# Kernel optimization log

Measured on AMD Instinct MI355X. Metric: run time of the kernel, lower is better.

Reference implementation:

```python
import jax, jax.numpy as jnp
import numpy as np

N = 50000      # nodes
E = 800000     # edges
D = 64         # model dim (in_dim == out_dim)
H = 8          # heads
Dh = D // H    # head dim = 8
CLAMP = 5.0
EPS_BN = 1e-5


def setup_inputs() -> dict:
    key = jax.random.key(0)
    ks = jax.random.split(key, 16)
    g = lambda i, shape, s=0.1: (jax.random.normal(ks[i], shape, jnp.float32) * s)
    z = lambda shape: jnp.zeros(shape, jnp.float32)
    o = lambda shape: jnp.ones(shape, jnp.float32)
    return dict(
        x=g(0, (N, D), 1.0),
        edge_attr=g(1, (E, D), 1.0),
        edge_index=jax.random.randint(ks[2], (2, E), 0, N, jnp.int32),
        Wq=g(3, (D, H * Dh)), bq=z((H * Dh,)),
        Wk=g(4, (D, H * Dh)),                      # K: use_bias=False (cfg default)
        We=g(5, (D, 2 * H * Dh)), be=z((2 * H * Dh,)),
        Wv=g(6, (D, H * Dh)),                      # V: use_bias=False
        Aw=g(7, (Dh, H, 1)),
        VeRow=g(8, (Dh, H, Dh)),
        deg_coef=g(9, (1, D, 2)),
        WOh=g(10, (D, D)), bOh=z((D,)),
        WOe=g(11, (D, D)), bOe=z((D,)),
        gamma1h=o((D,)), beta1h=z((D,)),
        gamma1e=o((D,)), beta1e=z((D,)),
        W1=g(12, (D, 2 * D)), b1=z((2 * D,)),
        W2=g(13, (2 * D, D)), b2=z((D,)),
        gamma2h=o((D,)), beta2h=z((D,)),
    )


def _bn(v, gamma, beta):
    # BatchNorm1d with batch statistics (training-mode math, biased var as in torch)
    mu = v.mean(axis=0)
    var = ((v - mu) ** 2).mean(axis=0)
    return (v - mu) * jax.lax.rsqrt(var + EPS_BN) * gamma + beta


def reference(x, edge_attr, edge_index, Wq, bq, Wk, We, be, Wv, Aw, VeRow,
              deg_coef, WOh, bOh, WOe, bOe, gamma1h, beta1h, gamma1e, beta1e,
              W1, b1, W2, b2, gamma2h, beta2h):
    src, dst = edge_index[0], edge_index[1]
    # degree scaler: deg computed on the fly from edge_index[1]
    deg = jax.ops.segment_sum(jnp.ones((E,), x.dtype), dst, num_segments=N)
    log_deg = jnp.log(deg + 1.0)[:, None]                       # [N,1]

    Q = (x @ Wq + bq).reshape(N, H, Dh)
    K = (x @ Wk).reshape(N, H, Dh)
    V = (x @ Wv).reshape(N, H, Dh)
    Ee = (edge_attr @ We + be).reshape(E, H, 2 * Dh)
    Ew, Eb = Ee[:, :, :Dh], Ee[:, :, Dh:]

    s = (K[src] + Q[dst]) * Ew                                  # [E,H,Dh]
    s = jnp.sqrt(jax.nn.relu(s)) - jnp.sqrt(jax.nn.relu(-s))    # signed sqrt
    s = jax.nn.relu(s + Eb)                                     # attn act = relu
    e_t = s
    wE = s.reshape(E, H * Dh)

    score = jnp.einsum('ehd,dhc->ehc', s, Aw)                   # [E,H,1]
    score = jnp.clip(score, -CLAMP, CLAMP)
    # segment softmax over destination nodes
    m = jax.ops.segment_max(score, dst, num_segments=N)
    m = jnp.where(jnp.isfinite(m), m, 0.0)
    ex = jnp.exp(score - m[dst])
    denom = jax.ops.segment_sum(ex, dst, num_segments=N)
    attn = ex / (denom[dst] + 1e-16)                            # [E,H,1]

    wV = jax.ops.segment_sum(V[src] * attn, dst, num_segments=N)    # [N,H,Dh]
    rowV = jax.ops.segment_sum(e_t * attn, dst, num_segments=N)     # [N,H,Dh]
    wV = wV + jnp.einsum('nhd,dhc->nhc', rowV, VeRow)

    h = wV.reshape(N, H * Dh)
    h = h * deg_coef[:, :, 0] + (h * log_deg) * deg_coef[:, :, 1]
    h = h @ WOh + bOh
    e = wE @ WOe + bOe

    h = _bn(x + h, gamma1h, beta1h)
    e = _bn(edge_attr + e, gamma1e, beta1e)

    h2 = jax.nn.relu(h @ W1 + b1) @ W2 + b2
    h = _bn(h + h2, gamma2h, beta2h)
    return h, e
```

## Files before the change

### kernel.cpp

```cpp
#include <hip/hip_runtime.h>
#include <hip/hip_bf16.h>

#define N_NODES 50000
#define N_EDGES 800000
#define CLAMP_V 5.0f
#define MAXDEG 64

typedef __hip_bfloat16 bf16;
typedef short s16x8 __attribute__((ext_vector_type(8)));
typedef float f32x4 __attribute__((ext_vector_type(4)));

__device__ __forceinline__ float b2f(bf16 v){ return __bfloat162float(v); }
__device__ __forceinline__ bf16 f2b(float v){ return __float2bfloat16(v); }

__device__ __forceinline__ float ldin(const void* p, size_t i, bool f32){
  return f32 ? ((const float*)p)[i] : b2f(((const bf16*)p)[i]);
}
__device__ __forceinline__ void stout(void* p, size_t i, float v, bool f32){
  if(f32) ((float*)p)[i]=v; else ((bf16*)p)[i]=f2b(v);
}
__device__ __forceinline__ void* e_region(void* d_out, bool f32){
  return f32 ? (void*)((float*)d_out + (size_t)N_NODES*64)
             : (void*)((bf16*)d_out + (size_t)N_NODES*64);
}

#define W_FLAG 0
#define W_DEG  64
#define W_ST   50064
#define W_ZEND 50448
#define W_BUCK 50448
#define W_QK   6450448
#define W_V    12850448
#define W_END  16050448
#define W_HV   W_QK
#define W_HPRE W_BUCK
#define W_HSUM (W_BUCK+3200000)

__global__ void detect_kernel(const unsigned short* __restrict__ wq_raw, unsigned* __restrict__ flag){
  int t=threadIdx.x; int cnt=0;
  for(int i=t;i<4096;i+=64){
    unsigned e=(wq_raw[i]>>7)&0xFF;
    if(e>=130) cnt++;
  }
  for(int o=32;o;o>>=1) cnt+=__shfl_down(cnt,o);
  if(t==0) *flag = (cnt>64)? 1u:0u;
}

__global__ __launch_bounds__(256) void build_kernel(const int* __restrict__ edge_index,
    unsigned* __restrict__ deg, uint2* __restrict__ buck2)
{
  int e = blockIdx.x*256+threadIdx.x;
  if(e < N_EDGES){
    int src = edge_index[e];
    int dst = edge_index[N_EDGES+e];
    unsigned j = atomicAdd(&deg[dst],1u);
    if(j < MAXDEG) buck2[(size_t)dst*MAXDEG + j] = make_uint2((unsigned)e,(unsigned)src);
  }
}

__global__ __launch_bounds__(256) void qkv_kernel(const void* __restrict__ x,
    const void* __restrict__ Wq, const void* __restrict__ bq,
    const void* __restrict__ Wk, const void* __restrict__ Wv,
    const unsigned* __restrict__ flagp, float* __restrict__ qk, float* __restrict__ vbuf)
{
  const bool f = (*flagp)!=0;
  __shared__ float sW[64*192];
  __shared__ float4 sxT[4][64];
  int t=threadIdx.x, wave=t>>6, lane=t&63;
  for (int i=t;i<64*64;i+=256){ int k=i>>6, j=i&63;
    sW[k*192+j]=ldin(Wq,i,f); sW[k*192+64+j]=ldin(Wk,i,f); sW[k*192+128+j]=ldin(Wv,i,f); }
  float bqv = ldin(bq,lane,f);
  __syncthreads();
  const int groups = N_NODES/16;
  const int stride = gridDim.x;
  int g = blockIdx.x;
  float cv0=0,cv1=0,cv2=0,cv3=0;
  if(g<groups){
    int n0=g*16+wave*4;
    cv0=ldin(x,(size_t)(n0+0)*64+lane,f);
    cv1=ldin(x,(size_t)(n0+1)*64+lane,f);
    cv2=ldin(x,(size_t)(n0+2)*64+lane,f);
    cv3=ldin(x,(size_t)(n0+3)*64+lane,f);
  }
  for (; g<groups; g+=stride){
    int n0 = g*16 + wave*4;
    sxT[wave][lane]=make_float4(cv0,cv1,cv2,cv3);
    int gn=g+stride; int gl = gn<groups?gn:g; int m0=gl*16+wave*4;
    float nv0=ldin(x,(size_t)(m0+0)*64+lane,f);
    float nv1=ldin(x,(size_t)(m0+1)*64+lane,f);
    float nv2=ldin(x,(size_t)(m0+2)*64+lane,f);
    float nv3=ldin(x,(size_t)(m0+3)*64+lane,f);
    float aq[4]={0,0,0,0}, ak[4]={0,0,0,0}, av[4]={0,0,0,0};
    #pragma unroll 8
    for(int k=0;k<64;k++){
      float4 a = sxT[wave][k];
      float w0=sW[k*192+lane], w1=sW[k*192+64+lane], w2=sW[k*192+128+lane];
      aq[0]+=a.x*w0; aq[1]+=a.y*w0; aq[2]+=a.z*w0; aq[3]+=a.w*w0;
      ak[0]+=a.x*w1; ak[1]+=a.y*w1; ak[2]+=a.z*w1; ak[3]+=a.w*w1;
      av[0]+=a.x*w2; av[1]+=a.y*w2; av[2]+=a.z*w2; av[3]+=a.w*w2;
    }
    #pragma unroll
    for(int r=0;r<4;r++){
      int n=n0+r;
      qk[n*128+lane]     = aq[r]+bqv;
      qk[n*128+64+lane]  = ak[r];
      vbuf[n*64+lane]    = av[r];
    }
    cv0=nv0; cv1=nv1; cv2=nv2; cv3=nv3;
  }
}

__global__ __launch_bounds__(256) void edgeA_kernel(
    const void* __restrict__ edge_attr, const int* __restrict__ edge_index,
    const void* __restrict__ We, const void* __restrict__ be,
    const float* __restrict__ qk, const unsigned* __restrict__ flagp, void* __restrict__ d_out)
{
  const bool f = (*flagp)!=0;
  void* s_buf = e_region(d_out,f);
  __shared__ float2 sWWB[64*64];
  __shared__ float4 seaT[4][64];
  int t=threadIdx.x, wave=t>>6, lane=t&63;
  int h=lane>>3, d=lane&7;
  for(int i=t;i<64*64;i+=256){ int k=i>>6, c=i&63; int hh=c>>3, dd=c&7;
    sWWB[i]=make_float2(ldin(We,(size_t)k*128+hh*16+dd,f),
                        ldin(We,(size_t)k*128+hh*16+8+dd,f)); }
  float beW=ldin(be,h*16+d,f), beB=ldin(be,h*16+8+d,f);
  __syncthreads();
  const int groups = N_EDGES/16;
  const int stride = gridDim.x;
  int g = blockIdx.x;
  if(g>=groups) return;
  float cv0,cv1,cv2,cv3; int cs0,cs1,cs2,cs3, cd0,cd1,cd2,cd3;
  {
    int e0=g*16+wave*4;
    cv0=ldin(edge_attr,(size_t)(e0+0)*64+lane,f);
    cv1=ldin(edge_attr,(size_t)(e0+1)*64+lane,f);
    cv2=ldin(edge_attr,(size_t)(e0+2)*64+lane,f);
    cv3=ldin(edge_attr,(size_t)(e0+3)*64+lane,f);
    cs0=edge_index[e0+0]; cs1=edge_index[e0+1]; cs2=edge_index[e0+2]; cs3=edge_index[e0+3];
    cd0=edge_index[N_EDGES+e0+0]; cd1=edge_index[N_EDGES+e0+1];
    cd2=edge_index[N_EDGES+e0+2]; cd3=edge_index[N_EDGES+e0+3];
  }
  for(; g<groups; g+=stride){
    int e0 = g*16 + wave*4;
    seaT[wave][lane]=make_float4(cv0,cv1,cv2,cv3);
    float kS0=qk[(size_t)cs0*128+64+lane], kD0=qk[(size_t)cd0*128+lane];
    float kS1=qk[(size_t)cs1*128+64+lane], kD1=qk[(size_t)cd1*128+lane];
    float kS2=qk[(size_t)cs2*128+64+lane], kD2=qk[(size_t)cd2*128+lane];
    float kS3=qk[(size_t)cs3*128+64+lane], kD3=qk[(size_t)cd3*128+lane];
    int gn=g+stride; int gl = gn<groups?gn:g; int m0=gl*16+wave*4;
    float nv0=ldin(edge_attr,(size_t)(m0+0)*64+lane,f);
    float nv1=ldin(edge_attr,(size_t)(m0+1)*64+lane,f);
    float nv2=ldin(edge_attr,(size_t)(m0+2)*64+lane,f);
    float nv3=ldin(edge_attr,(size_t)(m0+3)*64+lane,f);
    int ns0=edge_index[m0+0], ns1=edge_index[m0+1], ns2=edge_index[m0+2], ns3=edge_index[m0+3];
    int nd0=edge_index[N_EDGES+m0+0], nd1=edge_index[N_EDGES+m0+1];
    int nd2=edge_index[N_EDGES+m0+2], nd3=edge_index[N_EDGES+m0+3];
    float aW[4]={0,0,0,0}, aB[4]={0,0,0,0};
    #pragma unroll 8
    for(int k=0;k<64;k++){
      float4 a=seaT[wave][k];
      float2 w=sWWB[k*64+lane];
      aW[0]+=a.x*w.x; aB[0]+=a.x*w.y;
      aW[1]+=a.y*w.x; aB[1]+=a.y*w.y;
      aW[2]+=a.z*w.x; aB[2]+=a.z*w.y;
      aW[3]+=a.w*w.x; aB[3]+=a.w*w.y;
    }
    float kq0=kS0+kD0, kq1=kS1+kD1, kq2=kS2+kD2, kq3=kS3+kD3;
    {
      float Ew=aW[0]+beW, Eb=aB[0]+beB, s1=kq0*Ew;
      float s2=fmaxf(copysignf(sqrtf(fabsf(s1)),s1)+Eb,0.f);
      stout(s_buf,(size_t)(e0+0)*64+lane,s2,f);
    }
    {
      float Ew=aW[1]+beW, Eb=aB[1]+beB, s1=kq1*Ew;
      float s2=fmaxf(copysignf(sqrtf(fabsf(s1)),s1)+Eb,0.f);
      stout(s_buf,(size_t)(e0+1)*64+lane,s2,f);
    }
    {
      float Ew=aW[2]+beW, Eb=aB[2]+beB, s1=kq2*Ew;
      float s2=fmaxf(copysignf(sqrtf(fabsf(s1)),s1)+Eb,0.f);
      stout(s_buf,(size_t)(e0+2)*64+lane,s2,f);
    }
    {
      float Ew=aW[3]+beW, Eb=aB[3]+beB, s1=kq3*Ew;
      float s2=fmaxf(copysignf(sqrtf(fabsf(s1)),s1)+Eb,0.f);
      stout(s_buf,(size_t)(e0+3)*64+lane,s2,f);
    }
    cv0=nv0; cv1=nv1; cv2=nv2; cv3=nv3;
    cs0=ns0; cs1=ns1; cs2=ns2; cs3=ns3;
    cd0=nd0; cd1=nd1; cd2=nd2; cd3=nd3;
  }
}

__global__ __launch_bounds__(256) void gather_kernel(
    const unsigned* __restrict__ deg, const uint2* __restrict__ buck2,
    const void* __restrict__ Aw, const void* __restrict__ VeRow, const void* __restrict__ deg_coef,
    const float* __restrict__ vbuf, const unsigned* __restrict__ flagp,
    void* __restrict__ d_out, float* __restrict__ hv)
{
  const bool f = (*flagp)!=0;
  const void* s_buf = e_region(d_out,f);
  int t=threadIdx.x, wave=t>>6, lane=t&63;
  int h=lane>>3, d=lane&7;
  float awv = ldin(Aw, d*8+h, f);
  float ver[8];
  #pragma unroll
  for(int dd=0;dd<8;dd++) ver[dd]=ldin(VeRow,(dd*8+h)*8+d,f);
  float dc0=ldin(deg_coef,lane*2,f), dc1=ldin(deg_coef,lane*2+1,f);

  int n = blockIdx.x*4 + wave;
  unsigned degree = deg[n];
  int len = (int)(degree < MAXDEG ? degree : MAXDEG);
  const uint2* bk = &buck2[(size_t)n*MAXDEG];

  float den=0.f, wv=0.f, rv=0.f;
  for(int j=0;j<len;j+=4){
    float sv[4], vq[4]; int valid[4];
    #pragma unroll
    for(int i=0;i<4;i++){
      int jj=j+i; int js = jj<len ? jj : len-1;
      uint2 es = bk[js];
      sv[i]=ldin(s_buf,(size_t)es.x*64+lane,f);
      vq[i]=vbuf[(size_t)es.y*64+lane];
      valid[i]=(jj<len);
    }
    #pragma unroll
    for(int i=0;i<4;i++){
      float p = sv[i]*awv;
      p += __shfl_xor(p,1);
      p += __shfl_xor(p,2);
      p += __shfl_xor(p,4);
      p = fminf(fmaxf(p,-CLAMP_V),CLAMP_V);
      float ex = valid[i] ? __expf(p-CLAMP_V) : 0.f;
      den += ex; wv += vq[i]*ex; rv += sv[i]*ex;
    }
  }
  float inv = 1.f/(den + 1e-16f);
  wv *= inv; rv *= inv;
  float rvp=0.f;
  #pragma unroll
  for(int dd=0;dd<8;dd++){
    float rvd = __shfl(rv, (lane & 56) + dd);
    rvp += rvd * ver[dd];
  }
  float ld = __logf((float)degree + 1.f);
  hv[(size_t)n*64+lane] = (wv + rvp) * (dc0 + ld*dc1);
}

__global__ __launch_bounds__(256) void edgeD_kernel(const void* __restrict__ edge_attr,
    const void* __restrict__ WOe, const void* __restrict__ bOe,
    const unsigned* __restrict__ flagp, void* __restrict__ d_out, float* __restrict__ stats)
{
  const bool f = (*flagp)!=0;
  __shared__ float4 sm4[1536];
  float* sm=(float*)sm4;
  int t=threadIdx.x, wave=t>>6, lane=t&63;
  if(!f){
    bf16* eio = (bf16*)d_out + (size_t)N_NODES*64;
    const unsigned short* sb=(const unsigned short*)eio;
    unsigned short* BT=(unsigned short*)sm;
    float* red = sm + 2048;
    if(t<128) red[t]=0.f;
    for(int i=t;i<4096;i+=256){
      int j=i>>6, k=i&63;
      BT[(j*128+((k*2)^((j&7)<<4)))>>1]=((const unsigned short*)WOe)[(size_t)k*64+j];
    }
    __syncthreads();
    int qg=lane>>4, col=lane&15;
    s16x8 Bf[4][2];
    #pragma unroll
    for(int tl=0;tl<4;tl++){
      int j=tl*16+col;
      #pragma unroll
      for(int q=0;q<2;q++){
        int kb=qg*8+q*32;
        Bf[tl][q]=*(const s16x8*)((const char*)BT+j*128+((kb*2)^((j&7)<<4)));
      }
    }
    float boV[4];
    #pragma unroll
    for(int tl=0;tl<4;tl++) boV[tl]=b2f(((const bf16*)bOe)[tl*16+col]);
    float st1[4]={0,0,0,0}, st2[4]={0,0,0,0};
    f32x4 zz; zz[0]=0.f; zz[1]=0.f; zz[2]=0.f; zz[3]=0.f;
    const int groups=N_EDGES/64;
    for(int g=blockIdx.x; g<groups; g+=gridDim.x){
      int e0=g*64+wave*16, eq=e0+qg*4;
      const unsigned short* apr = sb + (size_t)(e0+col)*64 + qg*8;
      s16x8 A0=*(const s16x8*)apr;
      s16x8 A1=*(const s16x8*)(apr+32);
      f32x4 acc[4];
      #pragma unroll
      for(int tl=0;tl<4;tl++){
        acc[tl]=__builtin_amdgcn_mfma_f32_16x16x32_bf16(A0,Bf[tl][0],zz,0,0,0);
        acc[tl]=__builtin_amdgcn_mfma_f32_16x16x32_bf16(A1,Bf[tl][1],acc[tl],0,0,0);
      }
      #pragma unroll
      for(int r=0;r<4;r++){
        size_t eo=(size_t)(eq+r)*64;
        #pragma unroll
        for(int tl=0;tl<4;tl++){
          int c=tl*16+col;
          float ep=b2f(((const bf16*)edge_attr)[eo+c])+boV[tl]+acc[tl][r];
          eio[eo+c]=f2b(ep);
          st1[tl]+=ep; st2[tl]+=ep*ep;
        }
      }
    }
    #pragma unroll
    for(int tl=0;tl<4;tl++){
      int c=tl*16+col;
      atomicAdd(&red[c],st1[tl]);
      atomicAdd(&red[64+c],st2[tl]);
    }
    __syncthreads();
    if(t<128) atomicAdd(&stats[t],red[t]);
  } else {
    void* e_io = e_region(d_out,f);
    float* sW=sm; float4* sTa=(float4*)(sm+4096); float4* sTb=(float4*)(sm+5120);
    for(int i=t;i<64*64;i+=256) sW[i]=ldin(WOe,i,f);
    float bo=ldin(bOe,lane,f);
    float s1=0.f,s2=0.f;
    __syncthreads();
    const int groups=N_EDGES/32;
    for(int g=blockIdx.x;g<groups;g+=gridDim.x){
      int e0=g*32+wave*8;
      float v[8];
      #pragma unroll
      for(int r=0;r<8;r++) v[r]=ldin(e_io,(size_t)(e0+r)*64+lane,f);
      sTa[wave*64+lane]=make_float4(v[0],v[1],v[2],v[3]);
      sTb[wave*64+lane]=make_float4(v[4],v[5],v[6],v[7]);
      float acc[8]={0,0,0,0,0,0,0,0};
      #pragma unroll 8
      for(int k=0;k<64;k++){
        float4 a=sTa[wave*64+k], b=sTb[wave*64+k];
        float w=sW[k*64+lane];
        acc[0]+=a.x*w; acc[1]+=a.y*w; acc[2]+=a.z*w; acc[3]+=a.w*w;
        acc[4]+=b.x*w; acc[5]+=b.y*w; acc[6]+=b.z*w; acc[7]+=b.w*w;
      }
      #pragma unroll
      for(int r=0;r<8;r++){
        int e=e0+r;
        float ep=ldin(edge_attr,(size_t)e*64+lane,f)+bo+acc[r];
        stout(e_io,(size_t)e*64+lane,ep,f);
        s1+=ep; s2+=ep*ep;
      }
    }
    atomicAdd(&stats[lane], s1);
    atomicAdd(&stats[64+lane], s2);
  }
}

__global__ __launch_bounds__(256) void edgeE_kernel(const unsigned* __restrict__ flagp,
    void* __restrict__ d_out, const float* __restrict__ stats,
    const void* __restrict__ g1e, const void* __restrict__ b1e)
{
  const bool f = (*flagp)!=0;
  void* e_io = e_region(d_out,f);
  size_t tid=(size_t)blockIdx.x*256+threadIdx.x;
  int c=(int)(tid&63);
  float mu=stats[c]*(1.f/N_EDGES);
  float var=stats[64+c]*(1.f/N_EDGES)-mu*mu;
  float rs=rsqrtf(var+1e-5f);
  float val=ldin(e_io,tid,f);
  val=(val-mu)*rs*ldin(g1e,c,f)+ldin(b1e,c,f);
  stout(e_io,tid,val,f);
}

__global__ __launch_bounds__(256) void h1_kernel(const float* __restrict__ hv,
    const void* __restrict__ WOh, const void* __restrict__ bOh, const void* __restrict__ x,
    const unsigned* __restrict__ flagp, float* __restrict__ hpre, float* __restrict__ stats)
{
  const bool f = (*flagp)!=0;
  __shared__ float sW[64*64];
  __shared__ float4 sT[4][64];
  int t=threadIdx.x, wave=t>>6, lane=t&63;
  for(int i=t;i<64*64;i+=256) sW[i]=ldin(WOh,i,f);
  float bo=ldin(bOh,lane,f);
  float s1=0.f,s2=0.f;
  __syncthreads();
  const int groups=N_NODES/16;
  for(int g=blockIdx.x;g<groups;g+=gridDim.x){
    int n0=g*16+wave*4;
    sT[wave][lane]=make_float4(hv[(n0+0)*64+lane],hv[(n0+1)*64+lane],
                               hv[(n0+2)*64+lane],hv[(n0+3)*64+lane]);
    float acc[4]={0,0,0,0};
    #pragma unroll 8
    for(int k=0;k<64;k++){
      float4 a=sT[wave][k]; float w=sW[k*64+lane];
      acc[0]+=a.x*w; acc[1]+=a.y*w; acc[2]+=a.z*w; acc[3]+=a.w*w;
    }
    #pragma unroll
    for(int r=0;r<4;r++){
      int n=n0+r;
      float hp=ldin(x,(size_t)n*64+lane,f)+bo+acc[r];
      hpre[n*64+lane]=hp;
      s1+=hp; s2+=hp*hp;
    }
  }
  atomicAdd(&stats[128+lane],s1);
  atomicAdd(&stats[192+lane],s2);
}

__global__ __launch_bounds__(256) void h2_kernel(const float* __restrict__ hpre,
    const void* __restrict__ W1, const void* __restrict__ b1, const void* __restrict__ W2, const void* __restrict__ b2,
    const void* __restrict__ g1h, const void* __restrict__ be1h,
    const unsigned* __restrict__ flagp, float* __restrict__ hsum, float* __restrict__ stats)
{
  const bool f = (*flagp)!=0;
  __shared__ float sW1[64*128];
  __shared__ float4 shT[4][64];
  __shared__ float4 stT[4][128];
  int t=threadIdx.x, wave=t>>6, lane=t&63;
  for(int i=t;i<64*128;i+=256) sW1[i]=ldin(W1,i,f);
  float mu=stats[128+lane]*(1.f/N_NODES);
  float var=stats[192+lane]*(1.f/N_NODES)-mu*mu;
  float rs=rsqrtf(var+1e-5f);
  float gg=ldin(g1h,lane,f), bb=ldin(be1h,lane,f);
  float b1a=ldin(b1,lane,f), b1b=ldin(b1,64+lane,f);
  float b2c=ldin(b2,lane,f);
  float s1=0.f,s2=0.f;
  __syncthreads();
  const int groups=N_NODES/16;
  for(int g=blockIdx.x;g<groups;g+=gridDim.x){
    int n0=g*16+wave*4;
    float h1v[4];
    #pragma unroll
    for(int r=0;r<4;r++) h1v[r]=(hpre[(n0+r)*64+lane]-mu)*rs*gg+bb;
    shT[wave][lane]=make_float4(h1v[0],h1v[1],h1v[2],h1v[3]);
    float t0[4]={0,0,0,0}, t1[4]={0,0,0,0};
    #pragma unroll 8
    for(int k=0;k<64;k++){
      float4 a=shT[wave][k];
      float w0=sW1[k*128+lane], w1=sW1[k*128+64+lane];
      t0[0]+=a.x*w0; t0[1]+=a.y*w0; t0[2]+=a.z*w0; t0[3]+=a.w*w0;
      t1[0]+=a.x*w1; t1[1]+=a.y*w1; t1[2]+=a.z*w1; t1[3]+=a.w*w1;
    }
    #pragma unroll
    for(int r=0;r<4;r++){ t0[r]=fmaxf(t0[r]+b1a,0.f); t1[r]=fmaxf(t1[r]+b1b,0.f); }
    stT[wave][lane]=make_float4(t0[0],t0[1],t0[2],t0[3]);
    stT[wave][64+lane]=make_float4(t1[0],t1[1],t1[2],t1[3]);
    float acc[4]={0,0,0,0};
    #pragma unroll 8
    for(int k=0;k<128;k++){
      float4 a=stT[wave][k];
      float w=ldin(W2,(size_t)k*64+lane,f);
      acc[0]+=a.x*w; acc[1]+=a.y*w; acc[2]+=a.z*w; acc[3]+=a.w*w;
    }
    #pragma unroll
    for(int r=0;r<4;r++){
      float hs=h1v[r]+acc[r]+b2c;
      hsum[(n0+r)*64+lane]=hs;
      s1+=hs; s2+=hs*hs;
    }
  }
  atomicAdd(&stats[256+lane],s1);
  atomicAdd(&stats[320+lane],s2);
}

__global__ __launch_bounds__(256) void h3_kernel(const float* __restrict__ hsum,
    const float* __restrict__ stats, const void* __restrict__ g2h, const void* __restrict__ b2h,
    const unsigned* __restrict__ flagp, void* __restrict__ d_out)
{
  const bool f = (*flagp)!=0;
  int tid=blockIdx.x*256+threadIdx.x;
  int c=tid&63;
  float mu=stats[256+c]*(1.f/N_NODES);
  float var=stats[320+c]*(1.f/N_NODES)-mu*mu;
  float rs=rsqrtf(var+1e-5f);
  float val=(hsum[tid]-mu)*rs*ldin(g2h,c,f)+ldin(b2h,c,f);
  stout(d_out,tid,val,f);
}

extern "C" void kernel_launch(void* const* d_in, const int* in_sizes, int n_in,
                              void* d_out, int out_size, void* d_ws, size_t ws_size,
                              hipStream_t stream)
{
  const void* x        =d_in[0];
  const void* edge_attr=d_in[1];
  const int*  edge_index=(const int*)d_in[2];
  const void* Wq =d_in[3];
  const void* bq =d_in[4];
  const void* Wk =d_in[5];
  const void* We =d_in[6];
  const void* be =d_in[7];
  const void* Wv =d_in[8];
  const void* Aw =d_in[9];
  const void* VeRow=d_in[10];
  const void* deg_coef=d_in[11];
  const void* WOh=d_in[12];
  const void* bOh=d_in[13];
  const void* WOe=d_in[14];
  const void* bOe=d_in[15];
  const void* g1h=d_in[16];
  const void* be1h=d_in[17];
  const void* g1e=d_in[18];
  const void* be1e=d_in[19];
  const void* W1 =d_in[20];
  const void* b1 =d_in[21];
  const void* W2 =d_in[22];
  const void* b2 =d_in[23];
  const void* g2h=d_in[24];
  const void* be2h=d_in[25];

  float* ws=(float*)d_ws;
  unsigned* flag  =(unsigned*)(ws+W_FLAG);
  unsigned* deg   =(unsigned*)(ws+W_DEG);
  uint2*    buck2 =(uint2*)(ws+W_BUCK);
  float* stats=ws+W_ST;
  float* qk   =ws+W_QK;
  float* vbuf =ws+W_V;
  float* hv   =ws+W_HV;
  float* hpre =ws+W_HPRE;
  float* hsum =ws+W_HSUM;

  hipMemsetAsync(d_ws,0,(size_t)W_ZEND*4,stream);
  hipLaunchKernelGGL(detect_kernel,dim3(1),dim3(64),0,stream,(const unsigned short*)Wq,flag);
  hipLaunchKernelGGL(build_kernel, dim3(3125), dim3(256),0,stream, edge_index,deg,buck2);
  hipLaunchKernelGGL(qkv_kernel,   dim3(1024), dim3(256),0,stream, x,Wq,bq,Wk,Wv,flag,qk,vbuf);
  hipLaunchKernelGGL(edgeA_kernel, dim3(1024), dim3(256),0,stream, edge_attr,edge_index,We,be,qk,flag,d_out);
  hipLaunchKernelGGL(gather_kernel,dim3(12500),dim3(256),0,stream, deg,buck2,Aw,VeRow,deg_coef,vbuf,flag,d_out,hv);
  hipLaunchKernelGGL(edgeD_kernel, dim3(1024), dim3(256),0,stream, edge_attr,WOe,bOe,flag,d_out,stats);
  hipLaunchKernelGGL(edgeE_kernel, dim3(200000),dim3(256),0,stream, flag,d_out,stats,g1e,be1e);
  hipLaunchKernelGGL(h1_kernel,    dim3(1024), dim3(256),0,stream, hv,WOh,bOh,x,flag,hpre,stats);
  hipLaunchKernelGGL(h2_kernel,    dim3(1024), dim3(256),0,stream, hpre,W1,b1,W2,b2,g1h,be1h,flag,hsum,stats);
  hipLaunchKernelGGL(h3_kernel,    dim3(12500),dim3(256),0,stream, hsum,stats,g2h,be2h,flag,d_out);
}
```

Measured before the change: 1.417 ms.

## Fuse edge output projection into gather, merge kernels, add bf16 edge path

Folds the edge-bucket build into the QKV kernel, and splits edgeA into a bf16-specialised variant with packed bf16 weights in LDS plus an fp32 variant. The WOe projection and the edge BatchNorm statistics move into the gather kernel, which reuses the s values it already loads, with software-prefetched loads. The edge BN apply is merged into the h2 kernel as extra blocks, and h3 is vectorised. This removes separate passes over the edge tensor and several launches. In exchange, the MFMA edge projection becomes scalar FMA work in gather, and edges with a destination degree above MAXDEG would never get their output written.

```diff
diff --git a/kernel.cpp b/kernel.cpp
--- a/kernel.cpp
+++ b/kernel.cpp
@@ -7,11 +7,10 @@
 #define MAXDEG 64
 
 typedef __hip_bfloat16 bf16;
-typedef short s16x8 __attribute__((ext_vector_type(8)));
-typedef float f32x4 __attribute__((ext_vector_type(4)));
 
 __device__ __forceinline__ float b2f(bf16 v){ return __bfloat162float(v); }
 __device__ __forceinline__ bf16 f2b(float v){ return __float2bfloat16(v); }
+__device__ __forceinline__ unsigned short bbits(float v){ bf16 b=f2b(v); unsigned short u; __builtin_memcpy(&u,&b,2); return u; }
 
 __device__ __forceinline__ float ldin(const void* p, size_t i, bool f32){
   return f32 ? ((const float*)p)[i] : b2f(((const bf16*)p)[i]);
@@ -46,36 +45,35 @@
   if(t==0) *flag = (cnt>64)? 1u:0u;
 }
 
-__global__ __launch_bounds__(256) void build_kernel(const int* __restrict__ edge_index,
-    unsigned* __restrict__ deg, uint2* __restrict__ buck2)
-{
-  int e = blockIdx.x*256+threadIdx.x;
-  if(e < N_EDGES){
-    int src = edge_index[e];
-    int dst = edge_index[N_EDGES+e];
-    unsigned j = atomicAdd(&deg[dst],1u);
-    if(j < MAXDEG) buck2[(size_t)dst*MAXDEG + j] = make_uint2((unsigned)e,(unsigned)src);
-  }
-}
-
-__global__ __launch_bounds__(256) void qkv_kernel(const void* __restrict__ x,
+__global__ __launch_bounds__(256) void prep_kernel(const void* __restrict__ x,
     const void* __restrict__ Wq, const void* __restrict__ bq,
     const void* __restrict__ Wk, const void* __restrict__ Wv,
-    const unsigned* __restrict__ flagp, float* __restrict__ qk, float* __restrict__ vbuf)
-{
-  const bool f = (*flagp)!=0;
+    const unsigned* __restrict__ flagp, float* __restrict__ qk, float* __restrict__ vbuf,
+    const int* __restrict__ edge_index, unsigned* __restrict__ deg, uint2* __restrict__ buck2)
+{
   __shared__ float sW[64*192];
   __shared__ float4 sxT[4][64];
+  if(blockIdx.x>=1024){
+    int e=(blockIdx.x-1024)*256+threadIdx.x;
+    if(e<N_EDGES){
+      int src=edge_index[e];
+      int dst=edge_index[N_EDGES+e];
+      unsigned j=atomicAdd(&deg[dst],1u);
+      if(j<MAXDEG) buck2[(size_t)dst*MAXDEG+j]=make_uint2((unsigned)e,(unsigned)src);
+    }
+    return;
+  }
+  const bool f = (*flagp)!=0;
   int t=threadIdx.x, wave=t>>6, lane=t&63;
   for (int i=t;i<64*64;i+=256){ int k=i>>6, j=i&63;
     sW[k*192+j]=ldin(Wq,i,f); sW[k*192+64+j]=ldin(Wk,i,f); sW[k*192+128+j]=ldin(Wv,i,f); }
   float bqv = ldin(bq,lane,f);
   __syncthreads();
   const int groups = N_NODES/16;
-  const int stride = gridDim.x;
+  const int stride = 1024;
   int g = blockIdx.x;
   float cv0=0,cv1=0,cv2=0,cv3=0;
-  if(g<groups){
+  {
     int n0=g*16+wave*4;
     cv0=ldin(x,(size_t)(n0+0)*64+lane,f);
     cv1=ldin(x,(size_t)(n0+1)*64+lane,f);
@@ -110,12 +108,95 @@
   }
 }
 
-__global__ __launch_bounds__(256) void edgeA_kernel(
+__global__ __launch_bounds__(256) void edgeA_b(
     const void* __restrict__ edge_attr, const int* __restrict__ edge_index,
     const void* __restrict__ We, const void* __restrict__ be,
     const float* __restrict__ qk, const unsigned* __restrict__ flagp, void* __restrict__ d_out)
 {
-  const bool f = (*flagp)!=0;
+  if(*flagp) return;
+  bf16* s_out = (bf16*)d_out + (size_t)N_NODES*64;
+  const bf16* ea=(const bf16*)edge_attr;
+  __shared__ unsigned sWWB[64*64];
+  __shared__ float4 seaT[4][64];
+  int t=threadIdx.x, wave=t>>6, lane=t&63;
+  int h=lane>>3, d=lane&7;
+  const unsigned short* Wu=(const unsigned short*)We;
+  for(int i=t;i<64*64;i+=256){ int k=i>>6, c=i&63; int hh=c>>3, dd=c&7;
+    unsigned wb=Wu[(size_t)k*128+hh*16+dd], bb=Wu[(size_t)k*128+hh*16+8+dd];
+    sWWB[i]=wb|(bb<<16); }
+  float beW=b2f(((const bf16*)be)[h*16+d]), beB=b2f(((const bf16*)be)[h*16+8+d]);
+  __syncthreads();
+  const int groups = N_EDGES/16;
+  const int stride = gridDim.x;
+  int g = blockIdx.x;
+  float cv0,cv1,cv2,cv3; int cs0,cs1,cs2,cs3, cd0,cd1,cd2,cd3;
+  {
+    int e0=g*16+wave*4;
+    cv0=b2f(ea[(size_t)(e0+0)*64+lane]);
+    cv1=b2f(ea[(size_t)(e0+1)*64+lane]);
+    cv2=b2f(ea[(size_t)(e0+2)*64+lane]);
+    cv3=b2f(ea[(size_t)(e0+3)*64+lane]);
+    cs0=edge_index[e0+0]; cs1=edge_index[e0+1]; cs2=edge_index[e0+2]; cs3=edge_index[e0+3];
+    cd0=edge_index[N_EDGES+e0+0]; cd1=edge_index[N_EDGES+e0+1];
+    cd2=edge_index[N_EDGES+e0+2]; cd3=edge_index[N_EDGES+e0+3];
+  }
+  for(; g<groups; g+=stride){
+    int e0 = g*16 + wave*4;
+    seaT[wave][lane]=make_float4(cv0,cv1,cv2,cv3);
+    float kS0=qk[(size_t)cs0*128+64+lane], kD0=qk[(size_t)cd0*128+lane];
+    float kS1=qk[(size_t)cs1*128+64+lane], kD1=qk[(size_t)cd1*128+lane];
+    float kS2=qk[(size_t)cs2*128+64+lane], kD2=qk[(size_t)cd2*128+lane];
+    float kS3=qk[(size_t)cs3*128+64+lane], kD3=qk[(size_t)cd3*128+lane];
+    int gn=g+stride; int gl = gn<groups?gn:g; int m0=gl*16+wave*4;
+    float nv0=b2f(ea[(size_t)(m0+0)*64+lane]);
+    float nv1=b2f(ea[(size_t)(m0+1)*64+lane]);
+    float nv2=b2f(ea[(size_t)(m0+2)*64+lane]);
+    float nv3=b2f(ea[(size_t)(m0+3)*64+lane]);
+    int ns0=edge_index[m0+0], ns1=edge_index[m0+1], ns2=edge_index[m0+2], ns3=edge_index[m0+3];
+    int nd0=edge_index[N_EDGES+m0+0], nd1=edge_index[N_EDGES+m0+1];
+    int nd2=edge_index[N_EDGES+m0+2], nd3=edge_index[N_EDGES+m0+3];
+    float aW[4]={0,0,0,0}, aB[4]={0,0,0,0};
+    #pragma unroll 8
+    for(int k=0;k<64;k++){
+      float4 a=seaT[wave][k];
+      unsigned u=sWWB[k*64+lane];
+      float wx=__uint_as_float(u<<16);
+      float wy=__uint_as_float(u&0xFFFF0000u);
+      aW[0]+=a.x*wx; aB[0]+=a.x*wy;
+      aW[1]+=a.y*wx; aB[1]+=a.y*wy;
+      aW[2]+=a.z*wx; aB[2]+=a.z*wy;
+      aW[3]+=a.w*wx; aB[3]+=a.w*wy;
+    }
+    float kq0=kS0+kD0, kq1=kS1+kD1, kq2=kS2+kD2, kq3=kS3+kD3;
+    {
+      float Ew=aW[0]+beW, Eb=aB[0]+beB, s1=kq0*Ew;
+      s_out[(size_t)(e0+0)*64+lane]=f2b(fmaxf(copysignf(sqrtf(fabsf(s1)),s1)+Eb,0.f));
+    }
+    {
+      float Ew=aW[1]+beW, Eb=aB[1]+beB, s1=kq1*Ew;
+      s_out[(size_t)(e0+1)*64+lane]=f2b(fmaxf(copysignf(sqrtf(fabsf(s1)),s1)+Eb,0.f));
+    }
+    {
+      float Ew=aW[2]+beW, Eb=aB[2]+beB, s1=kq2*Ew;
+      s_out[(size_t)(e0+2)*64+lane]=f2b(fmaxf(copysignf(sqrtf(fabsf(s1)),s1)+Eb,0.f));
+    }
+    {
+      float Ew=aW[3]+beW, Eb=aB[3]+beB, s1=kq3*Ew;
+      s_out[(size_t)(e0+3)*64+lane]=f2b(fmaxf(copysignf(sqrtf(fabsf(s1)),s1)+Eb,0.f));
+    }
+    cv0=nv0; cv1=nv1; cv2=nv2; cv3=nv3;
+    cs0=ns0; cs1=ns1; cs2=ns2; cs3=ns3;
+    cd0=nd0; cd1=nd1; cd2=nd2; cd3=nd3;
+  }
+}
+
+__global__ __launch_bounds__(256) void edgeA_f(
+    const void* __restrict__ edge_attr, const int* __restrict__ edge_index,
+    const void* __restrict__ We, const void* __restrict__ be,
+    const float* __restrict__ qk, const unsigned* __restrict__ flagp, void* __restrict__ d_out)
+{
+  if(*flagp==0) return;
+  const bool f = true;
   void* s_buf = e_region(d_out,f);
   __shared__ float2 sWWB[64*64];
   __shared__ float4 seaT[4][64];
@@ -129,7 +210,6 @@
   const int groups = N_EDGES/16;
   const int stride = gridDim.x;
   int g = blockIdx.x;
-  if(g>=groups) return;
   float cv0,cv1,cv2,cv3; int cs0,cs1,cs2,cs3, cd0,cd1,cd2,cd3;
   {
     int e0=g*16+wave*4;
@@ -169,23 +249,19 @@
     float kq0=kS0+kD0, kq1=kS1+kD1, kq2=kS2+kD2, kq3=kS3+kD3;
     {
       float Ew=aW[0]+beW, Eb=aB[0]+beB, s1=kq0*Ew;
-      float s2=fmaxf(copysignf(sqrtf(fabsf(s1)),s1)+Eb,0.f);
-      stout(s_buf,(size_t)(e0+0)*64+lane,s2,f);
+      stout(s_buf,(size_t)(e0+0)*64+lane,fmaxf(copysignf(sqrtf(fabsf(s1)),s1)+Eb,0.f),f);
     }
     {
       float Ew=aW[1]+beW, Eb=aB[1]+beB, s1=kq1*Ew;
-      float s2=fmaxf(copysignf(sqrtf(fabsf(s1)),s1)+Eb,0.f);
-      stout(s_buf,(size_t)(e0+1)*64+lane,s2,f);
+      stout(s_buf,(size_t)(e0+1)*64+lane,fmaxf(copysignf(sqrtf(fabsf(s1)),s1)+Eb,0.f),f);
     }
     {
       float Ew=aW[2]+beW, Eb=aB[2]+beB, s1=kq2*Ew;
-      float s2=fmaxf(copysignf(sqrtf(fabsf(s1)),s1)+Eb,0.f);
-      stout(s_buf,(size_t)(e0+2)*64+lane,s2,f);
+      stout(s_buf,(size_t)(e0+2)*64+lane,fmaxf(copysignf(sqrtf(fabsf(s1)),s1)+Eb,0.f),f);
     }
     {
       float Ew=aW[3]+beW, Eb=aB[3]+beB, s1=kq3*Ew;
-      float s2=fmaxf(copysignf(sqrtf(fabsf(s1)),s1)+Eb,0.f);
-      stout(s_buf,(size_t)(e0+3)*64+lane,s2,f);
+      stout(s_buf,(size_t)(e0+3)*64+lane,fmaxf(copysignf(sqrtf(fabsf(s1)),s1)+Eb,0.f),f);
     }
     cv0=nv0; cv1=nv1; cv2=nv2; cv3=nv3;
     cs0=ns0; cs1=ns1; cs2=ns2; cs3=ns3;
@@ -196,35 +272,50 @@
 __global__ __launch_bounds__(256) void gather_kernel(
     const unsigned* __restrict__ deg, const uint2* __restrict__ buck2,
     const void* __restrict__ Aw, const void* __restrict__ VeRow, const void* __restrict__ deg_coef,
-    const float* __restrict__ vbuf, const unsigned* __restrict__ flagp,
-    void* __restrict__ d_out, float* __restrict__ hv)
+    const float* __restrict__ vbuf, const void* __restrict__ edge_attr,
+    const void* __restrict__ WOe, const void* __restrict__ bOe,
+    const unsigned* __restrict__ flagp,
+    void* __restrict__ d_out, float* __restrict__ hv, float* __restrict__ stats)
 {
   const bool f = (*flagp)!=0;
-  const void* s_buf = e_region(d_out,f);
+  void* e_io = e_region(d_out,f);
+  __shared__ float sWOe[64*64];
+  __shared__ float sS[4][4][64];
+  __shared__ float red[128];
   int t=threadIdx.x, wave=t>>6, lane=t&63;
   int h=lane>>3, d=lane&7;
+  for(int i=t;i<4096;i+=256) sWOe[i]=ldin(WOe,i,f);
+  if(t<128) red[t]=0.f;
   float awv = ldin(Aw, d*8+h, f);
   float ver[8];
   #pragma unroll
   for(int dd=0;dd<8;dd++) ver[dd]=ldin(VeRow,(dd*8+h)*8+d,f);
   float dc0=ldin(deg_coef,lane*2,f), dc1=ldin(deg_coef,lane*2+1,f);
+  float bo=ldin(bOe,lane,f);
+  __syncthreads();
 
   int n = blockIdx.x*4 + wave;
   unsigned degree = deg[n];
   int len = (int)(degree < MAXDEG ? degree : MAXDEG);
   const uint2* bk = &buck2[(size_t)n*MAXDEG];
 
-  float den=0.f, wv=0.f, rv=0.f;
+  float den=0.f, wv=0.f, rv=0.f, st1=0.f, st2=0.f;
+  unsigned ce[4]; float sv[4], vq[4], ea[4];
+  auto LB=[&](int j, unsigned* E_, float* S_, float* V_, float* A_){
+    #pragma unroll
+    for(int i=0;i<4;i++){
+      int js=j+i; if(js>len-1) js=len-1;
+      uint2 es=bk[js];
+      E_[i]=es.x;
+      S_[i]=ldin(e_io,(size_t)es.x*64+lane,f);
+      V_[i]=vbuf[(size_t)es.y*64+lane];
+      A_[i]=ldin(edge_attr,(size_t)es.x*64+lane,f);
+    }
+  };
+  if(len>0) LB(0,ce,sv,vq,ea);
   for(int j=0;j<len;j+=4){
-    float sv[4], vq[4]; int valid[4];
-    #pragma unroll
-    for(int i=0;i<4;i++){
-      int jj=j+i; int js = jj<len ? jj : len-1;
-      uint2 es = bk[js];
-      sv[i]=ldin(s_buf,(size_t)es.x*64+lane,f);
-      vq[i]=vbuf[(size_t)es.y*64+lane];
-      valid[i]=(jj<len);
-    }
+    unsigned ne[4]={0,0,0,0}; float nsv[4]={0,0,0,0}, nvq[4]={0,0,0,0}, nea[4]={0,0,0,0};
+    if(j+4<len) LB(j+4,ne,nsv,nvq,nea);
     #pragma unroll
     for(int i=0;i<4;i++){
       float p = sv[i]*awv;
@@ -232,9 +323,37 @@
       p += __shfl_xor(p,2);
       p += __shfl_xor(p,4);
       p = fminf(fmaxf(p,-CLAMP_V),CLAMP_V);
-      float ex = valid[i] ? __expf(p-CLAMP_V) : 0.f;
+      float ex = (j+i<len) ? __expf(p-CLAMP_V) : 0.f;
       den += ex; wv += vq[i]*ex; rv += sv[i]*ex;
     }
+    sS[wave][0][lane]=sv[0]; sS[wave][1][lane]=sv[1];
+    sS[wave][2][lane]=sv[2]; sS[wave][3][lane]=sv[3];
+    const float4* s0=(const float4*)sS[wave][0];
+    const float4* s1=(const float4*)sS[wave][1];
+    const float4* s2=(const float4*)sS[wave][2];
+    const float4* s3=(const float4*)sS[wave][3];
+    float a0=0.f,a1=0.f,a2=0.f,a3=0.f;
+    #pragma unroll 4
+    for(int k4=0;k4<16;k4++){
+      float4 x0=s0[k4], x1=s1[k4], x2=s2[k4], x3=s3[k4];
+      const float* wp=&sWOe[k4*256+lane];
+      float w0=wp[0], w1=wp[64], w2=wp[128], w3=wp[192];
+      a0+=x0.x*w0+x0.y*w1+x0.z*w2+x0.w*w3;
+      a1+=x1.x*w0+x1.y*w1+x1.z*w2+x1.w*w3;
+      a2+=x2.x*w0+x2.y*w1+x2.z*w2+x2.w*w3;
+      a3+=x3.x*w0+x3.y*w1+x3.z*w2+x3.w*w3;
+    }
+    float accs[4]={a0,a1,a2,a3};
+    #pragma unroll
+    for(int i=0;i<4;i++){
+      if(j+i<len){
+        float ep=ea[i]+bo+accs[i];
+        stout(e_io,(size_t)ce[i]*64+lane,ep,f);
+        st1+=ep; st2+=ep*ep;
+      }
+    }
+    #pragma unroll
+    for(int i=0;i<4;i++){ ce[i]=ne[i]; sv[i]=nsv[i]; vq[i]=nvq[i]; ea[i]=nea[i]; }
   }
   float inv = 1.f/(den + 1e-16f);
   wv *= inv; rv *= inv;
@@ -246,125 +365,10 @@
   }
   float ld = __logf((float)degree + 1.f);
   hv[(size_t)n*64+lane] = (wv + rvp) * (dc0 + ld*dc1);
-}
-
-__global__ __launch_bounds__(256) void edgeD_kernel(const void* __restrict__ edge_attr,
-    const void* __restrict__ WOe, const void* __restrict__ bOe,
-    const unsigned* __restrict__ flagp, void* __restrict__ d_out, float* __restrict__ stats)
-{
-  const bool f = (*flagp)!=0;
-  __shared__ float4 sm4[1536];
-  float* sm=(float*)sm4;
-  int t=threadIdx.x, wave=t>>6, lane=t&63;
-  if(!f){
-    bf16* eio = (bf16*)d_out + (size_t)N_NODES*64;
-    const unsigned short* sb=(const unsigned short*)eio;
-    unsigned short* BT=(unsigned short*)sm;
-    float* red = sm + 2048;
-    if(t<128) red[t]=0.f;
-    for(int i=t;i<4096;i+=256){
-      int j=i>>6, k=i&63;
-      BT[(j*128+((k*2)^((j&7)<<4)))>>1]=((const unsigned short*)WOe)[(size_t)k*64+j];
-    }
-    __syncthreads();
-    int qg=lane>>4, col=lane&15;
-    s16x8 Bf[4][2];
-    #pragma unroll
-    for(int tl=0;tl<4;tl++){
-      int j=tl*16+col;
-      #pragma unroll
-      for(int q=0;q<2;q++){
-        int kb=qg*8+q*32;
-        Bf[tl][q]=*(const s16x8*)((const char*)BT+j*128+((kb*2)^((j&7)<<4)));
-      }
-    }
-    float boV[4];
-    #pragma unroll
-    for(int tl=0;tl<4;tl++) boV[tl]=b2f(((const bf16*)bOe)[tl*16+col]);
-    float st1[4]={0,0,0,0}, st2[4]={0,0,0,0};
-    f32x4 zz; zz[0]=0.f; zz[1]=0.f; zz[2]=0.f; zz[3]=0.f;
-    const int groups=N_EDGES/64;
-    for(int g=blockIdx.x; g<groups; g+=gridDim.x){
-      int e0=g*64+wave*16, eq=e0+qg*4;
-      const unsigned short* apr = sb + (size_t)(e0+col)*64 + qg*8;
-      s16x8 A0=*(const s16x8*)apr;
-      s16x8 A1=*(const s16x8*)(apr+32);
-      f32x4 acc[4];
-      #pragma unroll
-      for(int tl=0;tl<4;tl++){
-        acc[tl]=__builtin_amdgcn_mfma_f32_16x16x32_bf16(A0,Bf[tl][0],zz,0,0,0);
-        acc[tl]=__builtin_amdgcn_mfma_f32_16x16x32_bf16(A1,Bf[tl][1],acc[tl],0,0,0);
-      }
-      #pragma unroll
-      for(int r=0;r<4;r++){
-        size_t eo=(size_t)(eq+r)*64;
-        #pragma unroll
-        for(int tl=0;tl<4;tl++){
-          int c=tl*16+col;
-          float ep=b2f(((const bf16*)edge_attr)[eo+c])+boV[tl]+acc[tl][r];
-          eio[eo+c]=f2b(ep);
-          st1[tl]+=ep; st2[tl]+=ep*ep;
-        }
-      }
-    }
-    #pragma unroll
-    for(int tl=0;tl<4;tl++){
-      int c=tl*16+col;
-      atomicAdd(&red[c],st1[tl]);
-      atomicAdd(&red[64+c],st2[tl]);
-    }
-    __syncthreads();
-    if(t<128) atomicAdd(&stats[t],red[t]);
-  } else {
-    void* e_io = e_region(d_out,f);
-    float* sW=sm; float4* sTa=(float4*)(sm+4096); float4* sTb=(float4*)(sm+5120);
-    for(int i=t;i<64*64;i+=256) sW[i]=ldin(WOe,i,f);
-    float bo=ldin(bOe,lane,f);
-    float s1=0.f,s2=0.f;
-    __syncthreads();
-    const int groups=N_EDGES/32;
-    for(int g=blockIdx.x;g<groups;g+=gridDim.x){
-      int e0=g*32+wave*8;
-      float v[8];
-      #pragma unroll
-      for(int r=0;r<8;r++) v[r]=ldin(e_io,(size_t)(e0+r)*64+lane,f);
-      sTa[wave*64+lane]=make_float4(v[0],v[1],v[2],v[3]);
-      sTb[wave*64+lane]=make_float4(v[4],v[5],v[6],v[7]);
-      float acc[8]={0,0,0,0,0,0,0,0};
-      #pragma unroll 8
-      for(int k=0;k<64;k++){
-        float4 a=sTa[wave*64+k], b=sTb[wave*64+k];
-        float w=sW[k*64+lane];
-        acc[0]+=a.x*w; acc[1]+=a.y*w; acc[2]+=a.z*w; acc[3]+=a.w*w;
-        acc[4]+=b.x*w; acc[5]+=b.y*w; acc[6]+=b.z*w; acc[7]+=b.w*w;
-      }
-      #pragma unroll
-      for(int r=0;r<8;r++){
-        int e=e0+r;
-        float ep=ldin(edge_attr,(size_t)e*64+lane,f)+bo+acc[r];
-        stout(e_io,(size_t)e*64+lane,ep,f);
-        s1+=ep; s2+=ep*ep;
-      }
-    }
-    atomicAdd(&stats[lane], s1);
-    atomicAdd(&stats[64+lane], s2);
-  }
-}
-
-__global__ __launch_bounds__(256) void edgeE_kernel(const unsigned* __restrict__ flagp,
-    void* __restrict__ d_out, const float* __restrict__ stats,
-    const void* __restrict__ g1e, const void* __restrict__ b1e)
-{
-  const bool f = (*flagp)!=0;
-  void* e_io = e_region(d_out,f);
-  size_t tid=(size_t)blockIdx.x*256+threadIdx.x;
-  int c=(int)(tid&63);
-  float mu=stats[c]*(1.f/N_EDGES);
-  float var=stats[64+c]*(1.f/N_EDGES)-mu*mu;
-  float rs=rsqrtf(var+1e-5f);
-  float val=ldin(e_io,tid,f);
-  val=(val-mu)*rs*ldin(g1e,c,f)+ldin(b1e,c,f);
-  stout(e_io,tid,val,f);
+  atomicAdd(&red[lane], st1);
+  atomicAdd(&red[64+lane], st2);
+  __syncthreads();
+  if(t<128) atomicAdd(&stats[t], red[t]);
 }
 
 __global__ __launch_bounds__(256) void h1_kernel(const float* __restrict__ hv,
@@ -402,16 +406,58 @@
   atomicAdd(&stats[192+lane],s2);
 }
 
-__global__ __launch_bounds__(256) void h2_kernel(const float* __restrict__ hpre,
+__global__ __launch_bounds__(256) void h2e_kernel(const float* __restrict__ hpre,
     const void* __restrict__ W1, const void* __restrict__ b1, const void* __restrict__ W2, const void* __restrict__ b2,
     const void* __restrict__ g1h, const void* __restrict__ be1h,
-    const unsigned* __restrict__ flagp, float* __restrict__ hsum, float* __restrict__ stats)
+    const void* __restrict__ g1e, const void* __restrict__ b1e,
+    const unsigned* __restrict__ flagp, float* __restrict__ hsum, float* __restrict__ stats,
+    void* __restrict__ d_out)
 {
   const bool f = (*flagp)!=0;
   __shared__ float sW1[64*128];
   __shared__ float4 shT[4][64];
   __shared__ float4 stT[4][128];
-  int t=threadIdx.x, wave=t>>6, lane=t&63;
+  int t=threadIdx.x;
+  if(blockIdx.x>=1024){
+    void* e_io = e_region(d_out,f);
+    float* A=sW1; float* B=sW1+64;
+    if(t<64){
+      float mu=stats[t]*(1.f/N_EDGES);
+      float var=stats[64+t]*(1.f/N_EDGES)-mu*mu;
+      float rs=rsqrtf(var+1e-5f);
+      float gg=ldin(g1e,t,f), bb=ldin(b1e,t,f);
+      A[t]=rs*gg; B[t]=bb-mu*rs*gg;
+    }
+    __syncthreads();
+    const size_t chunks=(size_t)N_EDGES*8;
+    size_t step=(size_t)(gridDim.x-1024)*256;
+    for(size_t ci=(size_t)(blockIdx.x-1024)*256+t; ci<chunks; ci+=step){
+      int cb=(int)((ci&7)*8);
+      if(!f){
+        uint4 v=((const uint4*)e_io)[ci];
+        unsigned r[4]={v.x,v.y,v.z,v.w}, o[4];
+        #pragma unroll
+        for(int q=0;q<4;q++){
+          float e0=__uint_as_float(r[q]<<16);
+          float e1=__uint_as_float(r[q]&0xFFFF0000u);
+          int c0=cb+q*2;
+          e0=e0*A[c0]+B[c0];
+          e1=e1*A[c0+1]+B[c0+1];
+          o[q]=(unsigned)bbits(e0) | ((unsigned)bbits(e1)<<16);
+        }
+        ((uint4*)e_io)[ci]=make_uint4(o[0],o[1],o[2],o[3]);
+      } else {
+        float4 v0=((const float4*)e_io)[ci*2], v1=((const float4*)e_io)[ci*2+1];
+        v0.x=v0.x*A[cb+0]+B[cb+0]; v0.y=v0.y*A[cb+1]+B[cb+1];
+        v0.z=v0.z*A[cb+2]+B[cb+2]; v0.w=v0.w*A[cb+3]+B[cb+3];
+        v1.x=v1.x*A[cb+4]+B[cb+4]; v1.y=v1.y*A[cb+5]+B[cb+5];
+        v1.z=v1.z*A[cb+6]+B[cb+6]; v1.w=v1.w*A[cb+7]+B[cb+7];
+        ((float4*)e_io)[ci*2]=v0; ((float4*)e_io)[ci*2+1]=v1;
+      }
+    }
+    return;
+  }
+  int wave=t>>6, lane=t&63;
   for(int i=t;i<64*128;i+=256) sW1[i]=ldin(W1,i,f);
   float mu=stats[128+lane]*(1.f/N_NODES);
   float var=stats[192+lane]*(1.f/N_NODES)-mu*mu;
@@ -422,7 +468,7 @@
   float s1=0.f,s2=0.f;
   __syncthreads();
   const int groups=N_NODES/16;
-  for(int g=blockIdx.x;g<groups;g+=gridDim.x){
+  for(int g=blockIdx.x;g<groups;g+=1024){
     int n0=g*16+wave*4;
     float h1v[4];
     #pragma unroll
@@ -464,12 +510,24 @@
 {
   const bool f = (*flagp)!=0;
   int tid=blockIdx.x*256+threadIdx.x;
-  int c=tid&63;
-  float mu=stats[256+c]*(1.f/N_NODES);
-  float var=stats[320+c]*(1.f/N_NODES)-mu*mu;
-  float rs=rsqrtf(var+1e-5f);
-  float val=(hsum[tid]-mu)*rs*ldin(g2h,c,f)+ldin(b2h,c,f);
-  stout(d_out,tid,val,f);
+  int c0=(tid&15)*4;
+  float4 v=((const float4*)hsum)[tid];
+  float o[4]={v.x,v.y,v.z,v.w};
+  #pragma unroll
+  for(int i=0;i<4;i++){
+    int c=c0+i;
+    float mu=stats[256+c]*(1.f/N_NODES);
+    float var=stats[320+c]*(1.f/N_NODES)-mu*mu;
+    float rs=rsqrtf(var+1e-5f);
+    o[i]=(o[i]-mu)*rs*ldin(g2h,c,f)+ldin(b2h,c,f);
+  }
+  if(!f){
+    unsigned lo=(unsigned)bbits(o[0]) | ((unsigned)bbits(o[1])<<16);
+    unsigned hi=(unsigned)bbits(o[2]) | ((unsigned)bbits(o[3])<<16);
+    ((uint2*)d_out)[tid]=make_uint2(lo,hi);
+  } else {
+    ((float4*)d_out)[tid]=make_float4(o[0],o[1],o[2],o[3]);
+  }
 }
 
 extern "C" void kernel_launch(void* const* d_in, const int* in_sizes, int n_in,
@@ -516,13 +574,14 @@
 
   hipMemsetAsync(d_ws,0,(size_t)W_ZEND*4,stream);
   hipLaunchKernelGGL(detect_kernel,dim3(1),dim3(64),0,stream,(const unsigned short*)Wq,flag);
-  hipLaunchKernelGGL(build_kernel, dim3(3125), dim3(256),0,stream, edge_index,deg,buck2);
-  hipLaunchKernelGGL(qkv_kernel,   dim3(1024), dim3(256),0,stream, x,Wq,bq,Wk,Wv,flag,qk,vbuf);
-  hipLaunchKernelGGL(edgeA_kernel, dim3(1024), dim3(256),0,stream, edge_attr,edge_index,We,be,qk,flag,d_out);
-  hipLaunchKernelGGL(gather_kernel,dim3(12500),dim3(256),0,stream, deg,buck2,Aw,VeRow,deg_coef,vbuf,flag,d_out,hv);
-  hipLaunchKernelGGL(edgeD_kernel, dim3(1024), dim3(256),0,stream, edge_attr,WOe,bOe,flag,d_out,stats);
-  hipLaunchKernelGGL(edgeE_kernel, dim3(200000),dim3(256),0,stream, flag,d_out,stats,g1e,be1e);
+  hipLaunchKernelGGL(prep_kernel,  dim3(1024+3125),dim3(256),0,stream,
+                     x,Wq,bq,Wk,Wv,flag,qk,vbuf,edge_index,deg,buck2);
+  hipLaunchKernelGGL(edgeA_b,      dim3(2048), dim3(256),0,stream, edge_attr,edge_index,We,be,qk,flag,d_out);
+  hipLaunchKernelGGL(edgeA_f,      dim3(1024), dim3(256),0,stream, edge_attr,edge_index,We,be,qk,flag,d_out);
+  hipLaunchKernelGGL(gather_kernel,dim3(12500),dim3(256),0,stream,
+                     deg,buck2,Aw,VeRow,deg_coef,vbuf,edge_attr,WOe,bOe,flag,d_out,hv,stats);
   hipLaunchKernelGGL(h1_kernel,    dim3(1024), dim3(256),0,stream, hv,WOh,bOh,x,flag,hpre,stats);
-  hipLaunchKernelGGL(h2_kernel,    dim3(1024), dim3(256),0,stream, hpre,W1,b1,W2,b2,g1h,be1h,flag,hsum,stats);
-  hipLaunchKernelGGL(h3_kernel,    dim3(12500),dim3(256),0,stream, hsum,stats,g2h,be2h,flag,d_out);
-}
+  hipLaunchKernelGGL(h2e_kernel,   dim3(3072), dim3(256),0,stream,
+                     hpre,W1,b1,W2,b2,g1h,be1h,g1e,be1e,flag,hsum,stats,d_out);
+  hipLaunchKernelGGL(h3_kernel,    dim3(3125), dim3(256),0,stream, hsum,stats,g2h,be2h,flag,d_out);
+}
```

After: 1.518 ms. +7.1%, slower.
